# Kernel tuning notes

Measured on AMD Instinct MI355X. Metric: run time of the kernel, lower is better.

The kernel has to match this reference:

```python
import jax, jax.numpy as jnp
import numpy as np

SCORE_THR = 0.005   # score_thres is None in init -> default 0.005
IOU_THR = 0.5
TOPK = 1024         # fixed pre-NMS candidate cap (JAX needs static shapes)


def setup_inputs() -> dict:
    key = jax.random.key(0)
    # (B, 4+nc, N_anchors): 16 images, 80 classes, 33600 anchors (1280x1280, strides 8/16/32)
    x = jax.random.normal(key, (16, 84, 33600), dtype=jnp.float32)
    return {"x": x}


def _pairwise_iou(b):
    # b: (K, 4) xyxy. Same math as torchvision.ops.box_iou.
    lt = jnp.maximum(b[:, None, :2], b[None, :, :2])   # (K, K, 2)
    rb = jnp.minimum(b[:, None, 2:], b[None, :, 2:])   # (K, K, 2)
    wh = jnp.clip(rb - lt, 0.0)
    inter = wh[..., 0] * wh[..., 1]
    area = (b[:, 2] - b[:, 0]) * (b[:, 3] - b[:, 1])
    union = area[:, None] + area[None, :] - inter
    return inter / jnp.maximum(union, 1e-9)


def _nms_single(boxes, svals, cids):
    # boxes (N,4); svals (N,) with -inf where score <= threshold; cids (N,) int
    top_s, idx = jax.lax.top_k(svals, TOPK)            # score-descending candidates
    b = boxes[idx]                                      # (K, 4)
    c = cids[idx]                                       # (K,)
    valid = top_s > SCORE_THR                           # thresholded-out slots are -inf
    iou = _pairwise_iou(b)                              # (K, K)
    ar = jnp.arange(TOPK)

    def body(i, keep):
        # greedy NMS: box i (if still kept) suppresses lower-scored boxes with IoU > thr
        sup = (iou[i] > IOU_THR) & (ar > i) & keep[i]
        return keep & ~sup

    keep = jax.lax.fori_loop(0, TOPK, body, valid)
    out = jnp.concatenate([b, top_s[:, None], c[:, None].astype(jnp.float32)], axis=1)  # (K, 6)
    out = jnp.where(keep[:, None], out, 0.0)            # padded fixed-size result
    return out, keep


def reference(x):
    xt = jnp.transpose(x, (0, 2, 1))                    # (B, N, 4+nc)
    boxes, scores = xt[..., :4], xt[..., 4:]
    svals = scores.max(-1)                              # (B, N)
    cids = scores.argmax(-1)                            # (B, N)
    svals = jnp.where(svals > SCORE_THR, svals, -jnp.inf)  # score-threshold mask
    out, keep = jax.vmap(_nms_single)(boxes, svals, cids)
    # out: (B, TOPK, 6) zero-padded [xyxy, score, cls]; keep: (B, TOPK) validity mask
    return out, keep
```

## Files before the change

kernel.cpp:

```cpp
#include <hip/hip_runtime.h>
#include <cstdint>
#include <cstddef>

#define NB 16
#define NC 84
#define NA 33600
#define NCLS 80
#define TOPK 1024
#define NBIN 8192
#define CANDCAP 8192
#define SCORE_THR 0.005f
#define IOU_THR 0.5f

__device__ __forceinline__ unsigned mono_u32(float f) {
    unsigned u = __float_as_uint(f);
    return (u & 0x80000000u) ? ~u : (u | 0x80000000u);
}
__device__ __forceinline__ float key_val(uint64_t k) {
    unsigned u = (unsigned)(k >> 32);
    u = (u & 0x80000000u) ? (u & 0x7FFFFFFFu) : ~u;
    return __uint_as_float(u);
}
__device__ __forceinline__ int key_idx(uint64_t k) {
    return (int)(~(uint32_t)(k & 0xFFFFFFFFu));
}

__global__ __launch_bounds__(256) void score_hist_kernel(const float* __restrict__ x,
                                                         float* __restrict__ sval,
                                                         int* __restrict__ cid,
                                                         unsigned* __restrict__ hist) {
    __shared__ unsigned h[NBIN];
    const int t = threadIdx.x;
    const int b = blockIdx.y;
    for (int i = t; i < NBIN; i += 256) h[i] = 0;
    __syncthreads();
    int q = blockIdx.x * 256 + t;
    if (q < NA / 4) {
        const float4* p = (const float4*)(x + (size_t)b * NC * NA + (size_t)4 * NA) + q;
        float4 best = p[0];
        int4 bc = {0, 0, 0, 0};
#pragma unroll 8
        for (int c = 1; c < NCLS; ++c) {
            float4 v = p[(size_t)c * (NA / 4)];
            if (v.x > best.x) { best.x = v.x; bc.x = c; }
            if (v.y > best.y) { best.y = v.y; bc.y = c; }
            if (v.z > best.z) { best.z = v.z; bc.z = c; }
            if (v.w > best.w) { best.w = v.w; bc.w = c; }
        }
        float4 s;
        s.x = (best.x > SCORE_THR) ? best.x : -INFINITY;
        s.y = (best.y > SCORE_THR) ? best.y : -INFINITY;
        s.z = (best.z > SCORE_THR) ? best.z : -INFINITY;
        s.w = (best.w > SCORE_THR) ? best.w : -INFINITY;
        ((float4*)sval)[(size_t)b * (NA / 4) + q] = s;
        ((int4*)cid)[(size_t)b * (NA / 4) + q] = bc;
        atomicAdd(&h[mono_u32(s.x) >> 19], 1u);
        atomicAdd(&h[mono_u32(s.y) >> 19], 1u);
        atomicAdd(&h[mono_u32(s.z) >> 19], 1u);
        atomicAdd(&h[mono_u32(s.w) >> 19], 1u);
    }
    __syncthreads();
    unsigned* gh = hist + (size_t)b * NBIN;
    for (int i = t; i < NBIN; i += 256) {
        unsigned v = h[i];
        if (v) atomicAdd(&gh[i], v);
    }
}

__global__ __launch_bounds__(256) void select_kernel(const float* __restrict__ sval,
                                                     const unsigned* __restrict__ hist,
                                                     uint64_t* __restrict__ cand,
                                                     unsigned* __restrict__ cnt) {
    __shared__ unsigned csum[256];
    __shared__ unsigned scut, lc, lbase;
    __shared__ uint64_t cbuf[2112];
    const int t = threadIdx.x;
    const int b = blockIdx.y;
    const int sl = blockIdx.x;

    const unsigned* gh = hist + (size_t)b * NBIN;
    unsigned cnts[32];
    unsigned local = 0;
#pragma unroll
    for (int q = 0; q < 32; ++q) {
        cnts[q] = gh[NBIN - 1 - (t * 32 + q)];
        local += cnts[q];
    }
    csum[t] = local;
    __syncthreads();
    for (int off = 1; off < 256; off <<= 1) {
        unsigned v = (t >= off) ? csum[t - off] : 0u;
        __syncthreads();
        csum[t] += v;
        __syncthreads();
    }
    unsigned incl = csum[t], excl = incl - local;
    if (excl < TOPK && incl >= TOPK) {
        unsigned cum = excl;
#pragma unroll
        for (int q = 0; q < 32; ++q) {
            if (cum + cnts[q] >= TOPK) { scut = (unsigned)(NBIN - 1 - (t * 32 + q)); break; }
            cum += cnts[q];
        }
    }
    if (t == 0) lc = 0;
    __syncthreads();
    unsigned cb = scut;

    int a0 = sl * (NA / 16);
    const float* sv = sval + (size_t)b * NA;
    for (int a = a0 + t; a < a0 + NA / 16; a += 256) {
        unsigned u = mono_u32(sv[a]);
        if ((u >> 19) >= cb) {
            unsigned pos = atomicAdd(&lc, 1u);
            cbuf[pos] = ((uint64_t)u << 32) | (uint32_t)(~(uint32_t)a);
        }
    }
    __syncthreads();
    if (t == 0) lbase = lc ? atomicAdd(&cnt[b * 64], lc) : 0u;
    __syncthreads();
    for (unsigned i = t; i < lc; i += 256) {
        unsigned p = lbase + i;
        if (p < CANDCAP) cand[((size_t)b << 13) + p] = cbuf[i];
    }
}

__global__ __launch_bounds__(256) void rank_gather_kernel(const float* __restrict__ x,
                                                          const int* __restrict__ cid,
                                                          const uint64_t* __restrict__ cand,
                                                          const unsigned* __restrict__ cnt,
                                                          float* __restrict__ tval,
                                                          float* __restrict__ bx1, float* __restrict__ by1,
                                                          float* __restrict__ bx2, float* __restrict__ by2,
                                                          float* __restrict__ barr, int* __restrict__ tcid) {
    __shared__ uint64_t lk[CANDCAP];
    const int t = threadIdx.x;
    const int b = blockIdx.y;
    const int sl = blockIdx.x;
    unsigned C = cnt[b * 64];
    if (C > CANDCAP) C = CANDCAP;
    const uint64_t* cb = cand + ((size_t)b << 13);
    for (unsigned i = t; i < C; i += 256) lk[i] = cb[i];
    __syncthreads();

    const int base = b << 10;
    const float* xb = x + (size_t)b * NC * NA;
    for (int i0 = sl * 256 + t; i0 < (int)C; i0 += 1024) {
        uint64_t my = lk[i0];
        unsigned rank = 0;
        int j = 0;
        for (; j + 4 <= (int)C; j += 4) {
            rank += (lk[j] > my);
            rank += (lk[j + 1] > my);
            rank += (lk[j + 2] > my);
            rank += (lk[j + 3] > my);
        }
        for (; j < (int)C; ++j) rank += (lk[j] > my);
        if (rank < TOPK) {
            int idx = key_idx(my);
            tval[base + rank] = key_val(my);
            float x1 = xb[idx], y1 = xb[NA + idx], x2 = xb[2 * NA + idx], y2 = xb[3 * NA + idx];
            bx1[base + rank] = x1; by1[base + rank] = y1;
            bx2[base + rank] = x2; by2[base + rank] = y2;
            barr[base + rank] = (x2 - x1) * (y2 - y1);
            tcid[base + rank] = cid[b * NA + idx];
        }
    }
}

#define LDSPAD(j) ((j) + ((j) >> 6))
__global__ __launch_bounds__(256) void mask_sweep_kernel(const float* __restrict__ tval,
                                                         const int* __restrict__ tcid,
                                                         const float* __restrict__ bx1,
                                                         const float* __restrict__ by1,
                                                         const float* __restrict__ bx2,
                                                         const float* __restrict__ by2,
                                                         const float* __restrict__ barr,
                                                         uint64_t* __restrict__ M,
                                                         int* __restrict__ rowflag,
                                                         unsigned* __restrict__ done,
                                                         float* __restrict__ out) {
    __shared__ float sx1[TOPK + 16], sy1[TOPK + 16], sx2[TOPK + 16], sy2[TOPK + 16], sar[TOPK + 16];
    __shared__ int anyf[256];
    __shared__ int list[TOPK];
    __shared__ unsigned sdone;
    const int t = threadIdx.x;
    const int b = blockIdx.y;
    const int base = b << 10;

    for (int j = t; j < TOPK; j += 256) {
        int ji = LDSPAD(j);
        sx1[ji] = bx1[base + j]; sy1[ji] = by1[base + j];
        sx2[ji] = bx2[base + j]; sy2[ji] = by2[base + j];
        sar[ji] = barr[base + j];
    }
    __syncthreads();

    int w = t & 15;
    int r = (blockIdx.x << 4) + (t >> 4);
    int ri = LDSPAD(r);
    float ix1 = sx1[ri], iy1 = sy1[ri], ix2 = sx2[ri], iy2 = sy2[ri], ia = sar[ri];
    uint64_t m = 0;
#pragma unroll 8
    for (int jj = 0; jj < 64; ++jj) {
        int j = (w << 6) + jj;
        int ji = w * 65 + jj;
        float ltx = fmaxf(ix1, sx1[ji]);
        float lty = fmaxf(iy1, sy1[ji]);
        float rbx = fminf(ix2, sx2[ji]);
        float rby = fminf(iy2, sy2[ji]);
        float ww = fmaxf(rbx - ltx, 0.0f);
        float hh = fmaxf(rby - lty, 0.0f);
        float inter = ww * hh;
        float uni = ia + sar[ji] - inter;
        float iou = inter / fmaxf(uni, 1e-9f);
        if (j > r && iou > IOU_THR) m |= (1ULL << jj);
    }
    M[(((size_t)(base + r)) << 4) + w] = m;
    anyf[t] = (m != 0ULL);
    __syncthreads();
    if (w == 0) {
        int any = 0;
#pragma unroll
        for (int q = 0; q < 16; ++q) any |= anyf[t + q];
        bool valid = tval[base + r] > SCORE_THR;
        rowflag[base + r] = (any && valid) ? 1 : 0;
    }

    __syncthreads();
    __threadfence();
    if (t == 0)
        sdone = __hip_atomic_fetch_add(&done[b], 1u, __ATOMIC_ACQ_REL, __HIP_MEMORY_SCOPE_AGENT);
    __syncthreads();
    if (sdone != 63) return;

    if (t >= 64) return;
    int l = t;
    int gg = l >> 4;
    w = l & 15;

    float tv[16];
#pragma unroll
    for (int s = 0; s < 16; ++s) tv[s] = tval[base + (s << 6) + l];

    uint64_t vword = 0;
#pragma unroll
    for (int s = 0; s < 16; ++s) {
        uint64_t bal = __ballot(tv[s] > SCORE_THR);
        if (l == s) vword = bal;
    }

    int cnt2 = 0;
#pragma unroll
    for (int s = 0; s < 16; ++s) {
        int flag = rowflag[base + (s << 6) + l];
        uint64_t mm = __ballot(flag != 0);
        if (flag) {
            int pos = cnt2 + __popcll(mm & ((1ULL << l) - 1ULL));
            list[pos] = (s << 6) + l;
        }
        cnt2 += __popcll(mm);
    }

    uint64_t remv = 0;
    for (int chunk = 0; chunk < cnt2; chunk += 64) {
        int mcnt = min(64, cnt2 - chunk);
        int idx_l = chunk + l;
        int myi = list[(idx_l < cnt2) ? idx_l : 0];
        uint64_t rows[16];
#pragma unroll
        for (int q = 0; q < 16; ++q) {
            int it = chunk + q * 4 + gg;
            int it2 = (it < cnt2) ? it : 0;
            uint64_t v = M[(((size_t)(base + list[it2])) << 4) + w];
            rows[q] = (it < cnt2) ? v : 0ULL;
        }
        for (int rr = 0; rr < mcnt; ++rr) {
            int i = __shfl(myi, rr, 64);
            uint64_t row = __shfl(rows[rr >> 2], ((rr & 3) << 4) + w, 64);
            uint64_t rb = __shfl(remv, i >> 6, 64);
            bool kept = !((rb >> (i & 63)) & 1ULL);
            remv |= (kept && l < 16) ? row : 0ULL;
        }
    }

    uint64_t kf = vword & ~remv;
#pragma unroll
    for (int s = 0; s < 16; ++s) {
        uint64_t kw = __shfl(kf, s, 64);
        bool kp = (kw >> l) & 1ULL;
        int k = (s << 6) + l;
        float x1 = bx1[base + k], y1 = by1[base + k];
        float x2 = bx2[base + k], y2 = by2[base + k];
        float* po = out + ((size_t)(base + k)) * 6;
        po[0] = kp ? x1 : 0.0f;
        po[1] = kp ? y1 : 0.0f;
        po[2] = kp ? x2 : 0.0f;
        po[3] = kp ? y2 : 0.0f;
        po[4] = kp ? tv[s] : 0.0f;
        po[5] = kp ? (float)tcid[base + k] : 0.0f;
        out[(size_t)NB * TOPK * 6 + base + k] = kp ? 1.0f : 0.0f;
    }
}

extern "C" void kernel_launch(void* const* d_in, const int* in_sizes, int n_in,
                              void* d_out, int out_size, void* d_ws, size_t ws_size,
                              hipStream_t stream) {
    const float* x = (const float*)d_in[0];
    float* out = (float*)d_out;
    char* ws = (char*)d_ws;

    size_t off = 0;
    auto alloc = [&](size_t bytes) { void* p = ws + off; off = (off + bytes + 255) & ~(size_t)255; return p; };
    float*    sval    = (float*)alloc((size_t)NB * NA * 4);
    int*      cid     = (int*)alloc((size_t)NB * NA * 4);
    unsigned* hist    = (unsigned*)alloc((size_t)NB * NBIN * 4);
    unsigned* cnt     = (unsigned*)alloc((size_t)NB * 64 * 4);
    unsigned* done    = (unsigned*)alloc(256);
    uint64_t* cand    = (uint64_t*)alloc((size_t)NB * CANDCAP * 8);
    float*    tval    = (float*)alloc((size_t)NB * TOPK * 4);
    float*    bx1     = (float*)alloc((size_t)NB * TOPK * 4);
    float*    by1     = (float*)alloc((size_t)NB * TOPK * 4);
    float*    bx2     = (float*)alloc((size_t)NB * TOPK * 4);
    float*    by2     = (float*)alloc((size_t)NB * TOPK * 4);
    float*    barr    = (float*)alloc((size_t)NB * TOPK * 4);
    int*      tcid    = (int*)alloc((size_t)NB * TOPK * 4);
    int*      rowflag = (int*)alloc((size_t)NB * TOPK * 4);
    uint64_t* M       = (uint64_t*)alloc((size_t)NB * TOPK * 16 * 8);

    size_t zbytes = (size_t)NB * NBIN * 4 + (size_t)NB * 64 * 4 + 256;
    hipMemsetAsync(hist, 0, zbytes, stream);

    score_hist_kernel<<<dim3(33, NB), 256, 0, stream>>>(x, sval, cid, hist);
    select_kernel<<<dim3(16, NB), 256, 0, stream>>>(sval, hist, cand, cnt);
    rank_gather_kernel<<<dim3(4, NB), 256, 0, stream>>>(x, cid, cand, cnt, tval,
                                                        bx1, by1, bx2, by2, barr, tcid);
    mask_sweep_kernel<<<dim3(64, NB), 256, 0, stream>>>(tval, tcid, bx1, by1, bx2, by2,
                                                        barr, M, rowflag, done, out);
}
```

Measured before the change: 433.5 us.

## Replace flagged-row list NMS sweep with blocked 64x64 diagonal-tile greedy resolve

The greedy suppression sweep no longer compacts rows with any overlap into a list and walks them serially with shuffles. It now processes the 1024 candidates in 16 blocks of 64. For each block it ORs in suppression from already-kept earlier blocks with a wave-wide xor reduction, then resolves the block with a scalar readlane loop over the diagonal tile. The per-image done counters are also padded to separate cache lines to avoid atomic contention. The new loop always runs 16x64 serial steps plus 120 off-diagonal loads per lane, whereas the old path scaled with the number of flagged rows.

Measured after the change: 478.6 us. 1.1x slower.

```diff
diff --git a/kernel.cpp b/kernel.cpp
--- a/kernel.cpp
+++ b/kernel.cpp
@@ -23,6 +23,14 @@
 }
 __device__ __forceinline__ int key_idx(uint64_t k) {
     return (int)(~(uint32_t)(k & 0xFFFFFFFFu));
+}
+__device__ __forceinline__ uint64_t readlane_u64(uint64_t v, int lane) {
+    unsigned lo = __builtin_amdgcn_readlane((unsigned)(v & 0xFFFFFFFFULL), lane);
+    unsigned hi = __builtin_amdgcn_readlane((unsigned)(v >> 32), lane);
+    return ((uint64_t)hi << 32) | (uint64_t)lo;
+}
+__device__ __forceinline__ uint64_t shfl_xor_u64(uint64_t v, int m) {
+    return (uint64_t)__shfl_xor((unsigned long long)v, m, 64);
 }
 
 __global__ __launch_bounds__(256) void score_hist_kernel(const float* __restrict__ x,
@@ -177,12 +185,9 @@
                                                          const float* __restrict__ by2,
                                                          const float* __restrict__ barr,
                                                          uint64_t* __restrict__ M,
-                                                         int* __restrict__ rowflag,
                                                          unsigned* __restrict__ done,
                                                          float* __restrict__ out) {
     __shared__ float sx1[TOPK + 16], sy1[TOPK + 16], sx2[TOPK + 16], sy2[TOPK + 16], sar[TOPK + 16];
-    __shared__ int anyf[256];
-    __shared__ int list[TOPK];
     __shared__ unsigned sdone;
     const int t = threadIdx.x;
     const int b = blockIdx.y;
@@ -196,99 +201,77 @@
     }
     __syncthreads();
 
-    int w = t & 15;
-    int r = (blockIdx.x << 4) + (t >> 4);
-    int ri = LDSPAD(r);
-    float ix1 = sx1[ri], iy1 = sy1[ri], ix2 = sx2[ri], iy2 = sy2[ri], ia = sar[ri];
-    uint64_t m = 0;
+    {
+        int w = t & 15;
+        int r = (blockIdx.x << 4) + (t >> 4);
+        int ri = LDSPAD(r);
+        float ix1 = sx1[ri], iy1 = sy1[ri], ix2 = sx2[ri], iy2 = sy2[ri], ia = sar[ri];
+        uint64_t m = 0;
 #pragma unroll 8
-    for (int jj = 0; jj < 64; ++jj) {
-        int j = (w << 6) + jj;
-        int ji = w * 65 + jj;
-        float ltx = fmaxf(ix1, sx1[ji]);
-        float lty = fmaxf(iy1, sy1[ji]);
-        float rbx = fminf(ix2, sx2[ji]);
-        float rby = fminf(iy2, sy2[ji]);
-        float ww = fmaxf(rbx - ltx, 0.0f);
-        float hh = fmaxf(rby - lty, 0.0f);
-        float inter = ww * hh;
-        float uni = ia + sar[ji] - inter;
-        float iou = inter / fmaxf(uni, 1e-9f);
-        if (j > r && iou > IOU_THR) m |= (1ULL << jj);
-    }
-    M[(((size_t)(base + r)) << 4) + w] = m;
-    anyf[t] = (m != 0ULL);
-    __syncthreads();
-    if (w == 0) {
-        int any = 0;
-#pragma unroll
-        for (int q = 0; q < 16; ++q) any |= anyf[t + q];
-        bool valid = tval[base + r] > SCORE_THR;
-        rowflag[base + r] = (any && valid) ? 1 : 0;
+        for (int jj = 0; jj < 64; ++jj) {
+            int j = (w << 6) + jj;
+            int ji = w * 65 + jj;
+            float ltx = fmaxf(ix1, sx1[ji]);
+            float lty = fmaxf(iy1, sy1[ji]);
+            float rbx = fminf(ix2, sx2[ji]);
+            float rby = fminf(iy2, sy2[ji]);
+            float ww = fmaxf(rbx - ltx, 0.0f);
+            float hh = fmaxf(rby - lty, 0.0f);
+            float inter = ww * hh;
+            float uni = ia + sar[ji] - inter;
+            float iou = inter / fmaxf(uni, 1e-9f);
+            if (j > r && iou > IOU_THR) m |= (1ULL << jj);
+        }
+        M[(((size_t)(base + r)) << 4) + w] = m;
     }
 
     __syncthreads();
     __threadfence();
     if (t == 0)
-        sdone = __hip_atomic_fetch_add(&done[b], 1u, __ATOMIC_ACQ_REL, __HIP_MEMORY_SCOPE_AGENT);
+        sdone = __hip_atomic_fetch_add(&done[b * 64], 1u, __ATOMIC_ACQ_REL, __HIP_MEMORY_SCOPE_AGENT);
     __syncthreads();
     if (sdone != 63) return;
 
     if (t >= 64) return;
-    int l = t;
-    int gg = l >> 4;
-    w = l & 15;
-
-    float tv[16];
-#pragma unroll
-    for (int s = 0; s < 16; ++s) tv[s] = tval[base + (s << 6) + l];
-
-    uint64_t vword = 0;
+    const int l = t;
+
+    float tvl[16];
+    uint64_t V[16], D[16], K[16];
+#pragma unroll
+    for (int q = 0; q < 16; ++q) {
+        tvl[q] = tval[base + (q << 6) + l];
+        V[q] = __ballot(tvl[q] > SCORE_THR);
+        D[q] = M[(((size_t)(base + (q << 6) + l)) << 4) + q];
+    }
+
+#pragma unroll
+    for (int q = 0; q < 16; ++q) {
+        uint64_t contrib = 0;
+#pragma unroll
+        for (int p = 0; p < 16; ++p) {
+            if (p < q) {
+                uint64_t cw = M[(((size_t)(base + (p << 6) + l)) << 4) + q];
+                contrib |= (((K[p] >> l) & 1ULL) ? cw : 0ULL);
+            }
+        }
+#pragma unroll
+        for (int s = 1; s < 64; s <<= 1) contrib |= shfl_xor_u64(contrib, s);
+        uint64_t rem = contrib;
+        uint64_t vq = V[q];
+        uint64_t Kq = 0;
+        for (int i = 0; i < 64; ++i) {
+            uint64_t row = readlane_u64(D[q], i);
+            uint64_t bit = 1ULL << i;
+            bool kept = ((vq & bit) != 0ULL) && ((rem & bit) == 0ULL);
+            rem |= kept ? row : 0ULL;
+            Kq |= kept ? bit : 0ULL;
+        }
+        K[q] = Kq;
+    }
+
 #pragma unroll
     for (int s = 0; s < 16; ++s) {
-        uint64_t bal = __ballot(tv[s] > SCORE_THR);
-        if (l == s) vword = bal;
-    }
-
-    int cnt2 = 0;
-#pragma unroll
-    for (int s = 0; s < 16; ++s) {
-        int flag = rowflag[base + (s << 6) + l];
-        uint64_t mm = __ballot(flag != 0);
-        if (flag) {
-            int pos = cnt2 + __popcll(mm & ((1ULL << l) - 1ULL));
-            list[pos] = (s << 6) + l;
-        }
-        cnt2 += __popcll(mm);
-    }
-
-    uint64_t remv = 0;
-    for (int chunk = 0; chunk < cnt2; chunk += 64) {
-        int mcnt = min(64, cnt2 - chunk);
-        int idx_l = chunk + l;
-        int myi = list[(idx_l < cnt2) ? idx_l : 0];
-        uint64_t rows[16];
-#pragma unroll
-        for (int q = 0; q < 16; ++q) {
-            int it = chunk + q * 4 + gg;
-            int it2 = (it < cnt2) ? it : 0;
-            uint64_t v = M[(((size_t)(base + list[it2])) << 4) + w];
-            rows[q] = (it < cnt2) ? v : 0ULL;
-        }
-        for (int rr = 0; rr < mcnt; ++rr) {
-            int i = __shfl(myi, rr, 64);
-            uint64_t row = __shfl(rows[rr >> 2], ((rr & 3) << 4) + w, 64);
-            uint64_t rb = __shfl(remv, i >> 6, 64);
-            bool kept = !((rb >> (i & 63)) & 1ULL);
-            remv |= (kept && l < 16) ? row : 0ULL;
-        }
-    }
-
-    uint64_t kf = vword & ~remv;
-#pragma unroll
-    for (int s = 0; s < 16; ++s) {
-        uint64_t kw = __shfl(kf, s, 64);
-        bool kp = (kw >> l) & 1ULL;
+        bool kp = (K[s] >> l) & 1ULL;
         int k = (s << 6) + l;
         float x1 = bx1[base + k], y1 = by1[base + k];
         float x2 = bx2[base + k], y2 = by2[base + k];
@@ -297,7 +280,7 @@
         po[1] = kp ? y1 : 0.0f;
         po[2] = kp ? x2 : 0.0f;
         po[3] = kp ? y2 : 0.0f;
-        po[4] = kp ? tv[s] : 0.0f;
+        po[4] = kp ? tvl[s] : 0.0f;
         po[5] = kp ? (float)tcid[base + k] : 0.0f;
         out[(size_t)NB * TOPK * 6 + base + k] = kp ? 1.0f : 0.0f;
     }
@@ -316,7 +299,7 @@
     int*      cid     = (int*)alloc((size_t)NB * NA * 4);
     unsigned* hist    = (unsigned*)alloc((size_t)NB * NBIN * 4);
     unsigned* cnt     = (unsigned*)alloc((size_t)NB * 64 * 4);
-    unsigned* done    = (unsigned*)alloc(256);
+    unsigned* done    = (unsigned*)alloc((size_t)NB * 64 * 4);
     uint64_t* cand    = (uint64_t*)alloc((size_t)NB * CANDCAP * 8);
     float*    tval    = (float*)alloc((size_t)NB * TOPK * 4);
     float*    bx1     = (float*)alloc((size_t)NB * TOPK * 4);
@@ -325,10 +308,9 @@
     float*    by2     = (float*)alloc((size_t)NB * TOPK * 4);
     float*    barr    = (float*)alloc((size_t)NB * TOPK * 4);
     int*      tcid    = (int*)alloc((size_t)NB * TOPK * 4);
-    int*      rowflag = (int*)alloc((size_t)NB * TOPK * 4);
     uint64_t* M       = (uint64_t*)alloc((size_t)NB * TOPK * 16 * 8);
 
-    size_t zbytes = (size_t)NB * NBIN * 4 + (size_t)NB * 64 * 4 + 256;
+    size_t zbytes = (size_t)NB * NBIN * 4 + (size_t)NB * 64 * 4 * 2;
     hipMemsetAsync(hist, 0, zbytes, stream);
 
     score_hist_kernel<<<dim3(33, NB), 256, 0, stream>>>(x, sval, cid, hist);
@@ -336,5 +318,5 @@
     rank_gather_kernel<<<dim3(4, NB), 256, 0, stream>>>(x, cid, cand, cnt, tval,
                                                         bx1, by1, bx2, by2, barr, tcid);
     mask_sweep_kernel<<<dim3(64, NB), 256, 0, stream>>>(tval, tcid, bx1, by1, bx2, by2,
-                                                        barr, M, rowflag, done, out);
-}
+                                                        barr, M, done, out);
+}
```
